# Kernel tuning notes

Hardware: AMD Instinct MI355X
Metric: run time of the kernel (lower is better)

The kernel has to match this reference:

```python
import jax, jax.numpy as jnp
import numpy as np

N, P, C = 2_000_000, 64, 100


def setup_inputs() -> dict:
    key = jax.random.key(0)
    k1, k2 = jax.random.split(key)
    x = jax.random.normal(k1, (N, P), dtype=jnp.float32)
    t = jax.random.randint(k2, (N,), 0, C, dtype=jnp.int64)
    return {"x": x, "t": t, "num_classes": C}


def reference(x, t, num_classes):
    # trace(cov(cla.T)) == sum of per-feature unbiased variances of rows with t==j.
    # Compute per-class count / sum / sum-of-squares with one fused segment reduce
    # instead of forming a p x p covariance per class.
    t = t.astype(jnp.int32)
    counts = jax.ops.segment_sum(jnp.ones((x.shape[0],), x.dtype), t,
                                 num_segments=num_classes)          # [C]
    s = jax.ops.segment_sum(x, t, num_segments=num_classes)          # [C, P]
    ss = jax.ops.segment_sum(x * x, t, num_segments=num_classes)     # [C, P]
    n = counts[:, None]
    # unbiased variance (torch.cov default correction=1): (E[x^2]*n - (sum)^2/n)/(n-1)
    var = (ss - s * s / n) / (n - 1.0)                               # [C, P]
    vc = jnp.sum(var)
    return jnp.reshape(vc / num_classes, (1,))
```

## Files before the change

kernel.cpp:

```cpp
#include <hip/hip_runtime.h>

#define NFEAT 64
#define NCLS  100
#define ACC   (NCLS * NFEAT)
#define NB    512
#define ABLK  256
#define AGRID 2048

#define OFF_GS    0
#define OFF_GSS   6400
#define OFF_GCNT  12800
#define OFF_CB    12928
#define OFF_BCNT  13056
#define OFF_ORDER (13056 + NB * NCLS)

__global__ void zero_ws_kernel(float* ws) {
    int i = blockIdx.x * blockDim.x + threadIdx.x;
    if (i < 2 * ACC + NCLS) ws[i] = 0.0f;
}

__global__ __launch_bounds__(256, 4)
void hist_kernel(const int* __restrict__ t, unsigned* __restrict__ bcnt,
                 unsigned* __restrict__ gcnt, int n, int chunk) {
    __shared__ unsigned h[NCLS];
    for (int i = threadIdx.x; i < NCLS; i += 256) h[i] = 0u;
    __syncthreads();
    const int b = blockIdx.x, s = b * chunk, e = min(n, s + chunk);
    for (int i = s + threadIdx.x; i < e; i += 256) atomicAdd(&h[t[i]], 1u);
    __syncthreads();
    for (int c = threadIdx.x; c < NCLS; c += 256) {
        bcnt[b * NCLS + c] = h[c];
        atomicAdd(&gcnt[c], h[c]);
    }
}

__global__ void prefix_kernel(const unsigned* __restrict__ gcnt,
                              unsigned* __restrict__ cb,
                              unsigned* __restrict__ bcnt, int n) {
    if (threadIdx.x == 0) {
        unsigned r = 0;
        for (int c = 0; c < NCLS; c++) { cb[c] = r; r += gcnt[c]; }
        cb[NCLS] = r;
    }
    __syncthreads();
    const int c = threadIdx.x;
    if (c < NCLS) {
        unsigned run = cb[c];
        for (int b = 0; b < NB; b++) {
            unsigned v = bcnt[b * NCLS + c];
            bcnt[b * NCLS + c] = run;
            run += v;
        }
    }
}

__global__ __launch_bounds__(256, 4)
void scatter_kernel(const int* __restrict__ t, const unsigned* __restrict__ bcnt,
                    int* __restrict__ order, int n, int chunk) {
    __shared__ unsigned cur[NCLS];
    const int b = blockIdx.x;
    for (int c = threadIdx.x; c < NCLS; c += 256) cur[c] = bcnt[b * NCLS + c];
    __syncthreads();
    const int s = b * chunk, e = min(n, s + chunk);
    for (int i = s + threadIdx.x; i < e; i += 256) {
        const int c = t[i];
        const unsigned p = atomicAdd(&cur[c], 1u);
        order[p] = i;
    }
}

__global__ __launch_bounds__(ABLK, 8)
void accum_sorted(const float* __restrict__ x, const int* __restrict__ order,
                  const unsigned* __restrict__ cb_g,
                  float* __restrict__ gs, float* __restrict__ gss,
                  int n, int ch) {
    __shared__ unsigned cb[NCLS + 1];
    for (int i = threadIdx.x; i < NCLS + 1; i += ABLK) cb[i] = cb_g[i];
    __syncthreads();

    const int lane = threadIdx.x & 63;
    const int gw = blockIdx.x * (ABLK / 64) + (threadIdx.x >> 6);
    long long i0 = (long long)gw * ch;
    long long i1 = min((long long)n, i0 + ch);
    if (i0 >= i1) return;

    int lo = 0, hi = NCLS - 1;
    while (lo < hi) {
        const int mid = (lo + hi + 1) >> 1;
        if ((long long)cb[mid] <= i0) lo = mid; else hi = mid - 1;
    }
    int c = lo;

    while (i0 < i1 && c < NCLS) {
        const long long segEnd = min(i1, (long long)cb[c + 1]);
        if (segEnd > i0) {
            float s = 0.0f, ss = 0.0f;
            long long i = i0;
            for (; i + 8 <= segEnd; i += 8) {
                const int* op = order + i;
                int r[8];
#pragma unroll
                for (int u = 0; u < 8; u++) r[u] = __builtin_amdgcn_readfirstlane(op[u]);
                float v[8];
#pragma unroll
                for (int u = 0; u < 8; u++) v[u] = x[(long long)r[u] * NFEAT + lane];
#pragma unroll
                for (int u = 0; u < 8; u++) { s += v[u]; ss += v[u] * v[u]; }
            }
            for (; i < segEnd; i++) {
                const int r = __builtin_amdgcn_readfirstlane(order[i]);
                const float v = x[(long long)r * NFEAT + lane];
                s += v; ss += v * v;
            }
            const int base = c * NFEAT + lane;
            unsafeAtomicAdd(&gs[base], s);
            unsafeAtomicAdd(&gss[base], ss);
        }
        i0 = segEnd; c++;
    }
}

__global__ void finalize_kernel(const float* __restrict__ gs,
                                const float* __restrict__ gss,
                                const unsigned int* __restrict__ gcnt,
                                float* __restrict__ out) {
    __shared__ double red[256];
    double acc = 0.0;
    for (int i = threadIdx.x; i < ACC; i += 256) {
        const int c = i >> 6;
        const double n  = (double)gcnt[c];
        const double s  = (double)gs[i];
        const double ss = (double)gss[i];
        acc += (ss - s * s / n) / (n - 1.0);
    }
    red[threadIdx.x] = acc;
    __syncthreads();
    for (int off = 128; off > 0; off >>= 1) {
        if (threadIdx.x < off) red[threadIdx.x] += red[threadIdx.x + off];
        __syncthreads();
    }
    if (threadIdx.x == 0) out[0] = (float)(red[0] / (double)NCLS);
}

__global__ __launch_bounds__(1024, 8)
void accum_fallback(const float* __restrict__ x, const int* __restrict__ t,
                    float* __restrict__ gs, float* __restrict__ gss, int nrows) {
    __shared__ float ls[ACC];
    __shared__ float lss[ACC];
    const int tid = threadIdx.x;
    for (int i = tid; i < ACC; i += 1024) { ls[i] = 0.0f; lss[i] = 0.0f; }
    __syncthreads();
    const int lane = tid & 63, wave = tid >> 6;
    const long long step = (long long)512 * 16 * 8;
    long long row0 = ((long long)blockIdx.x * 16 + wave) * 8;
    for (; row0 + 8 <= nrows; row0 += step) {
        const int* tp = t + row0;
        const float* xp = x + row0 * NFEAT + lane;
        int c[8]; float v[8];
#pragma unroll
        for (int u = 0; u < 8; u++) c[u] = __builtin_amdgcn_readfirstlane(tp[u]);
#pragma unroll
        for (int u = 0; u < 8; u++) v[u] = xp[u * NFEAT];
#pragma unroll
        for (int u = 0; u < 8; u++) {
            const int base = c[u] * NFEAT + lane;
            unsafeAtomicAdd(&ls[base], v[u]);
            unsafeAtomicAdd(&lss[base], v[u] * v[u]);
        }
    }
    for (; row0 < nrows; row0++) {
        const int c = __builtin_amdgcn_readfirstlane(t[row0]);
        const float v = x[row0 * NFEAT + lane];
        unsafeAtomicAdd(&ls[c * NFEAT + lane], v);
        unsafeAtomicAdd(&lss[c * NFEAT + lane], v * v);
    }
    __syncthreads();
    for (int i = tid; i < ACC; i += 1024) {
        unsafeAtomicAdd(&gs[i], ls[i]);
        unsafeAtomicAdd(&gss[i], lss[i]);
    }
}

extern "C" void kernel_launch(void* const* d_in, const int* in_sizes, int n_in,
                              void* d_out, int out_size, void* d_ws, size_t ws_size,
                              hipStream_t stream) {
    const float* x = (const float*)d_in[0];
    const int*   t = (const int*)d_in[1];
    const int n = in_sizes[1];

    float*    wsf  = (float*)d_ws;
    unsigned* wsu  = (unsigned*)d_ws;
    float*    gs   = wsf + OFF_GS;
    float*    gss  = wsf + OFF_GSS;
    unsigned* gcnt = wsu + OFF_GCNT;
    unsigned* cb   = wsu + OFF_CB;
    unsigned* bcnt = wsu + OFF_BCNT;
    int*      order = (int*)(wsu + OFF_ORDER);

    const size_t needed = (size_t)(OFF_ORDER + n) * 4;
    const int zwords = 2 * ACC + NCLS;
    zero_ws_kernel<<<(zwords + 255) / 256, 256, 0, stream>>>((float*)d_ws);

    if (ws_size >= needed) {
        const int chunk = (n + NB - 1) / NB;
        hist_kernel<<<NB, 256, 0, stream>>>(t, bcnt, gcnt, n, chunk);
        prefix_kernel<<<1, 128, 0, stream>>>(gcnt, cb, bcnt, n);
        scatter_kernel<<<NB, 256, 0, stream>>>(t, bcnt, order, n, chunk);
        const int nw = AGRID * (ABLK / 64);
        const int ch = (n + nw - 1) / nw;
        accum_sorted<<<AGRID, ABLK, 0, stream>>>(x, order, cb, gs, gss, n, ch);
    } else {
        const int chunk = (n + NB - 1) / NB;
        hist_kernel<<<NB, 256, 0, stream>>>(t, bcnt, gcnt, n, chunk);
        accum_fallback<<<512, 1024, 0, stream>>>(x, t, gs, gss, n);
    }
    finalize_kernel<<<1, 256, 0, stream>>>(gs, gss, gcnt, (float*)d_out);
}
```

Before: 718.9 us.

## Replace sort-based segment reduction with fused single-pass LDS accumulation

Removes the histogram/prefix/scatter/gather pipeline and instead streams x and t once, accumulating per-class sums, sums of squares and counts in shared memory with LDS atomics. Per-block partials are written to workspace and reduced deterministically in double by a separate kernel, avoiding global float atomics. This eliminates the extra passes over t and the order array and the random row gather, at the cost of heavy LDS atomic traffic and a partials buffer write/read.

```diff
diff --git a/kernel.cpp b/kernel.cpp
--- a/kernel.cpp
+++ b/kernel.cpp
@@ -3,121 +3,103 @@
 #define NFEAT 64
 #define NCLS  100
 #define ACC   (NCLS * NFEAT)
-#define NB    512
-#define ABLK  256
-#define AGRID 2048
+#define FBLK  512
+#define FTHR  1024
 
 #define OFF_GS    0
 #define OFF_GSS   6400
 #define OFF_GCNT  12800
-#define OFF_CB    12928
-#define OFF_BCNT  13056
-#define OFF_ORDER (13056 + NB * NCLS)
+#define OFF_PART  12928
 
-__global__ void zero_ws_kernel(float* ws) {
+__global__ void zero_u32_kernel(unsigned* __restrict__ p, int n) {
     int i = blockIdx.x * blockDim.x + threadIdx.x;
-    if (i < 2 * ACC + NCLS) ws[i] = 0.0f;
+    if (i < n) p[i] = 0u;
 }
 
-__global__ __launch_bounds__(256, 4)
-void hist_kernel(const int* __restrict__ t, unsigned* __restrict__ bcnt,
-                 unsigned* __restrict__ gcnt, int n, int chunk) {
-    __shared__ unsigned h[NCLS];
-    for (int i = threadIdx.x; i < NCLS; i += 256) h[i] = 0u;
+__global__ __launch_bounds__(FTHR, 8)
+void fused_accum(const float* __restrict__ x, const int* __restrict__ t,
+                 float* __restrict__ partials,
+                 float* __restrict__ gs, float* __restrict__ gss,
+                 unsigned* __restrict__ gcnt, int n, int atomic_flush) {
+    __shared__ float ls[ACC];
+    __shared__ float lss[ACC];
+    __shared__ unsigned lcnt[NCLS];
+    const int tid = threadIdx.x;
+    for (int i = tid; i < ACC; i += FTHR) { ls[i] = 0.f; lss[i] = 0.f; }
+    if (tid < NCLS) lcnt[tid] = 0u;
     __syncthreads();
-    const int b = blockIdx.x, s = b * chunk, e = min(n, s + chunk);
-    for (int i = s + threadIdx.x; i < e; i += 256) atomicAdd(&h[t[i]], 1u);
+
+    const int lane = tid & 63;
+    const int wave = tid >> 6;
+    const long long step = (long long)FBLK * (FTHR / 64) * 8;
+    long long row0 = ((long long)blockIdx.x * (FTHR / 64) + wave) * 8;
+
+    for (; row0 + 8 <= n; row0 += step) {
+        const int*   tp = t + row0;
+        const float* xp = x + row0 * NFEAT + lane;
+        int c[8]; float v[8];
+#pragma unroll
+        for (int u = 0; u < 8; u++) c[u] = __builtin_amdgcn_readfirstlane(tp[u]);
+#pragma unroll
+        for (int u = 0; u < 8; u++) v[u] = xp[u * NFEAT];
+
+        int myc = c[0];
+        if (lane == 1) myc = c[1];
+        if (lane == 2) myc = c[2];
+        if (lane == 3) myc = c[3];
+        if (lane == 4) myc = c[4];
+        if (lane == 5) myc = c[5];
+        if (lane == 6) myc = c[6];
+        if (lane == 7) myc = c[7];
+        if (lane < 8) atomicAdd(&lcnt[myc], 1u);
+
+#pragma unroll
+        for (int u = 0; u < 8; u++) {
+            const int base = c[u] * NFEAT + lane;
+            unsafeAtomicAdd(&ls[base],  v[u]);
+            unsafeAtomicAdd(&lss[base], v[u] * v[u]);
+        }
+    }
+    for (; row0 < n; row0++) {
+        const int c0 = __builtin_amdgcn_readfirstlane(t[row0]);
+        const float vv = x[row0 * NFEAT + lane];
+        unsafeAtomicAdd(&ls[c0 * NFEAT + lane],  vv);
+        unsafeAtomicAdd(&lss[c0 * NFEAT + lane], vv * vv);
+        if (lane == 0) atomicAdd(&lcnt[c0], 1u);
+    }
     __syncthreads();
-    for (int c = threadIdx.x; c < NCLS; c += 256) {
-        bcnt[b * NCLS + c] = h[c];
-        atomicAdd(&gcnt[c], h[c]);
+
+    if (atomic_flush) {
+        for (int i = tid; i < ACC; i += FTHR) {
+            unsafeAtomicAdd(&gs[i],  ls[i]);
+            unsafeAtomicAdd(&gss[i], lss[i]);
+        }
+    } else {
+        float* pb = partials + (size_t)blockIdx.x * (2 * ACC);
+        for (int i = tid; i < ACC; i += FTHR) {
+            pb[i]       = ls[i];
+            pb[ACC + i] = lss[i];
+        }
+    }
+    if (tid < NCLS) {
+        const unsigned vv = lcnt[tid];
+        if (vv) atomicAdd(&gcnt[tid], vv);
     }
 }
 
-__global__ void prefix_kernel(const unsigned* __restrict__ gcnt,
-                              unsigned* __restrict__ cb,
-                              unsigned* __restrict__ bcnt, int n) {
-    if (threadIdx.x == 0) {
-        unsigned r = 0;
-        for (int c = 0; c < NCLS; c++) { cb[c] = r; r += gcnt[c]; }
-        cb[NCLS] = r;
+__global__ __launch_bounds__(256)
+void reduce_partials(const float* __restrict__ part, float* __restrict__ gsgss) {
+    const int j = blockIdx.x * 256 + threadIdx.x;
+    if (j >= 2 * ACC) return;
+    const float* p = part + j;
+    double a0 = 0.0, a1 = 0.0, a2 = 0.0, a3 = 0.0;
+    for (int b = 0; b < FBLK; b += 4) {
+        a0 += (double)p[(size_t)(b + 0) * (2 * ACC)];
+        a1 += (double)p[(size_t)(b + 1) * (2 * ACC)];
+        a2 += (double)p[(size_t)(b + 2) * (2 * ACC)];
+        a3 += (double)p[(size_t)(b + 3) * (2 * ACC)];
     }
-    __syncthreads();
-    const int c = threadIdx.x;
-    if (c < NCLS) {
-        unsigned run = cb[c];
-        for (int b = 0; b < NB; b++) {
-            unsigned v = bcnt[b * NCLS + c];
-            bcnt[b * NCLS + c] = run;
-            run += v;
-        }
-    }
-}
-
-__global__ __launch_bounds__(256, 4)
-void scatter_kernel(const int* __restrict__ t, const unsigned* __restrict__ bcnt,
-                    int* __restrict__ order, int n, int chunk) {
-    __shared__ unsigned cur[NCLS];
-    const int b = blockIdx.x;
-    for (int c = threadIdx.x; c < NCLS; c += 256) cur[c] = bcnt[b * NCLS + c];
-    __syncthreads();
-    const int s = b * chunk, e = min(n, s + chunk);
-    for (int i = s + threadIdx.x; i < e; i += 256) {
-        const int c = t[i];
-        const unsigned p = atomicAdd(&cur[c], 1u);
-        order[p] = i;
-    }
-}
-
-__global__ __launch_bounds__(ABLK, 8)
-void accum_sorted(const float* __restrict__ x, const int* __restrict__ order,
-                  const unsigned* __restrict__ cb_g,
-                  float* __restrict__ gs, float* __restrict__ gss,
-                  int n, int ch) {
-    __shared__ unsigned cb[NCLS + 1];
-    for (int i = threadIdx.x; i < NCLS + 1; i += ABLK) cb[i] = cb_g[i];
-    __syncthreads();
-
-    const int lane = threadIdx.x & 63;
-    const int gw = blockIdx.x * (ABLK / 64) + (threadIdx.x >> 6);
-    long long i0 = (long long)gw * ch;
-    long long i1 = min((long long)n, i0 + ch);
-    if (i0 >= i1) return;
-
-    int lo = 0, hi = NCLS - 1;
-    while (lo < hi) {
-        const int mid = (lo + hi + 1) >> 1;
-        if ((long long)cb[mid] <= i0) lo = mid; else hi = mid - 1;
-    }
-    int c = lo;
-
-    while (i0 < i1 && c < NCLS) {
-        const long long segEnd = min(i1, (long long)cb[c + 1]);
-        if (segEnd > i0) {
-            float s = 0.0f, ss = 0.0f;
-            long long i = i0;
-            for (; i + 8 <= segEnd; i += 8) {
-                const int* op = order + i;
-                int r[8];
-#pragma unroll
-                for (int u = 0; u < 8; u++) r[u] = __builtin_amdgcn_readfirstlane(op[u]);
-                float v[8];
-#pragma unroll
-                for (int u = 0; u < 8; u++) v[u] = x[(long long)r[u] * NFEAT + lane];
-#pragma unroll
-                for (int u = 0; u < 8; u++) { s += v[u]; ss += v[u] * v[u]; }
-            }
-            for (; i < segEnd; i++) {
-                const int r = __builtin_amdgcn_readfirstlane(order[i]);
-                const float v = x[(long long)r * NFEAT + lane];
-                s += v; ss += v * v;
-            }
-            const int base = c * NFEAT + lane;
-            unsafeAtomicAdd(&gs[base], s);
-            unsafeAtomicAdd(&gss[base], ss);
-        }
-        i0 = segEnd; c++;
-    }
+    gsgss[j] = (float)((a0 + a1) + (a2 + a3));
 }
 
 __global__ void finalize_kernel(const float* __restrict__ gs,
@@ -142,45 +124,6 @@
     if (threadIdx.x == 0) out[0] = (float)(red[0] / (double)NCLS);
 }
 
-__global__ __launch_bounds__(1024, 8)
-void accum_fallback(const float* __restrict__ x, const int* __restrict__ t,
-                    float* __restrict__ gs, float* __restrict__ gss, int nrows) {
-    __shared__ float ls[ACC];
-    __shared__ float lss[ACC];
-    const int tid = threadIdx.x;
-    for (int i = tid; i < ACC; i += 1024) { ls[i] = 0.0f; lss[i] = 0.0f; }
-    __syncthreads();
-    const int lane = tid & 63, wave = tid >> 6;
-    const long long step = (long long)512 * 16 * 8;
-    long long row0 = ((long long)blockIdx.x * 16 + wave) * 8;
-    for (; row0 + 8 <= nrows; row0 += step) {
-        const int* tp = t + row0;
-        const float* xp = x + row0 * NFEAT + lane;
-        int c[8]; float v[8];
-#pragma unroll
-        for (int u = 0; u < 8; u++) c[u] = __builtin_amdgcn_readfirstlane(tp[u]);
-#pragma unroll
-        for (int u = 0; u < 8; u++) v[u] = xp[u * NFEAT];
-#pragma unroll
-        for (int u = 0; u < 8; u++) {
-            const int base = c[u] * NFEAT + lane;
-            unsafeAtomicAdd(&ls[base], v[u]);
-            unsafeAtomicAdd(&lss[base], v[u] * v[u]);
-        }
-    }
-    for (; row0 < nrows; row0++) {
-        const int c = __builtin_amdgcn_readfirstlane(t[row0]);
-        const float v = x[row0 * NFEAT + lane];
-        unsafeAtomicAdd(&ls[c * NFEAT + lane], v);
-        unsafeAtomicAdd(&lss[c * NFEAT + lane], v * v);
-    }
-    __syncthreads();
-    for (int i = tid; i < ACC; i += 1024) {
-        unsafeAtomicAdd(&gs[i], ls[i]);
-        unsafeAtomicAdd(&gss[i], lss[i]);
-    }
-}
-
 extern "C" void kernel_launch(void* const* d_in, const int* in_sizes, int n_in,
                               void* d_out, int out_size, void* d_ws, size_t ws_size,
                               hipStream_t stream) {
@@ -193,26 +136,18 @@
     float*    gs   = wsf + OFF_GS;
     float*    gss  = wsf + OFF_GSS;
     unsigned* gcnt = wsu + OFF_GCNT;
-    unsigned* cb   = wsu + OFF_CB;
-    unsigned* bcnt = wsu + OFF_BCNT;
-    int*      order = (int*)(wsu + OFF_ORDER);
+    float*    part = wsf + OFF_PART;
 
-    const size_t needed = (size_t)(OFF_ORDER + n) * 4;
-    const int zwords = 2 * ACC + NCLS;
-    zero_ws_kernel<<<(zwords + 255) / 256, 256, 0, stream>>>((float*)d_ws);
+    const size_t needed = ((size_t)OFF_PART + (size_t)FBLK * 2 * ACC) * 4;
 
     if (ws_size >= needed) {
-        const int chunk = (n + NB - 1) / NB;
-        hist_kernel<<<NB, 256, 0, stream>>>(t, bcnt, gcnt, n, chunk);
-        prefix_kernel<<<1, 128, 0, stream>>>(gcnt, cb, bcnt, n);
-        scatter_kernel<<<NB, 256, 0, stream>>>(t, bcnt, order, n, chunk);
-        const int nw = AGRID * (ABLK / 64);
-        const int ch = (n + nw - 1) / nw;
-        accum_sorted<<<AGRID, ABLK, 0, stream>>>(x, order, cb, gs, gss, n, ch);
+        zero_u32_kernel<<<1, 128, 0, stream>>>(gcnt, NCLS);
+        fused_accum<<<FBLK, FTHR, 0, stream>>>(x, t, part, gs, gss, gcnt, n, 0);
+        reduce_partials<<<(2 * ACC + 255) / 256, 256, 0, stream>>>(part, wsf);
+        finalize_kernel<<<1, 256, 0, stream>>>(gs, gss, gcnt, (float*)d_out);
     } else {
-        const int chunk = (n + NB - 1) / NB;
-        hist_kernel<<<NB, 256, 0, stream>>>(t, bcnt, gcnt, n, chunk);
-        accum_fallback<<<512, 1024, 0, stream>>>(x, t, gs, gss, n);
+        zero_u32_kernel<<<(12900 + 255) / 256, 256, 0, stream>>>(wsu, 2 * ACC + NCLS);
+        fused_accum<<<FBLK, FTHR, 0, stream>>>(x, t, nullptr, gs, gss, gcnt, n, 1);
+        finalize_kernel<<<1, 256, 0, stream>>>(gs, gss, gcnt, (float*)d_out);
     }
-    finalize_kernel<<<1, 256, 0, stream>>>(gs, gss, gcnt, (float*)d_out);
 }
```

Result: slower. 1.820 ms (+153.1%).
